# Kernel optimization log

Measured on AMD Instinct MI355X. Metric: run time of the kernel, lower is better.

Reference implementation:

```python
import jax, jax.numpy as jnp
import numpy as np

IN_DIM, HID, MEM, OUT = 512, 1024, 1024, 512
BATCH = 4096
HIST = 5  # hist_steps hard-coded in MMU.__init__

_LINEARS = [("inpgate", IN_DIM, HID), ("rec_inpgate", OUT, HID), ("mem_inpgate", MEM, HID),
            ("inp", IN_DIM, HID), ("rec_inp", OUT, HID),
            ("readgate", IN_DIM, MEM), ("rec_readgate", OUT, MEM), ("mem_readgate", MEM, MEM),
            ("decoder", HID, MEM),
            ("writegate", IN_DIM, MEM), ("rec_writegate", OUT, MEM), ("mem_writegate", MEM, MEM),
            ("encoder", MEM, HID)]


def setup_inputs() -> dict:
    key = jax.random.key(0)
    ks = iter(jax.random.split(key, 2 * len(_LINEARS) + 4))
    d = {"input": jax.random.normal(next(ks), (IN_DIM, BATCH), jnp.float32)}
    for name, fin, fout in _LINEARS:
        bound = 1.0 / np.sqrt(fin)  # torch nn.Linear default init range
        d["W_" + name] = jax.random.uniform(next(ks), (fout, fin), jnp.float32, -bound, bound)
        d["b_" + name] = jax.random.uniform(next(ks), (fout,), jnp.float32, -bound, bound)
    d["w_hid_out"] = jax.random.uniform(next(ks), (OUT, MEM), jnp.float32)  # torch.rand
    return d


def reference(input, W_inpgate, b_inpgate, W_rec_inpgate, b_rec_inpgate,
              W_mem_inpgate, b_mem_inpgate, W_inp, b_inp, W_rec_inp, b_rec_inp,
              W_readgate, b_readgate, W_rec_readgate, b_rec_readgate,
              W_mem_readgate, b_mem_readgate, W_decoder, b_decoder,
              W_writegate, b_writegate, W_rec_writegate, b_rec_writegate,
              W_mem_writegate, b_mem_writegate, W_encoder, b_encoder, w_hid_out):
    B = input.shape[1]
    lin = lambda x, W, b: x @ W.T + b
    # fresh module: history is zeros except last slot = current input (transposed to [B, in])
    xs = jnp.concatenate([jnp.zeros((HIST - 1, B, IN_DIM), input.dtype), input.T[None]], axis=0)

    def step(carry, x):
        out, mem = carry  # [B, OUT], [B, MEM]
        block_inp = jax.nn.sigmoid(lin(x, W_inp, b_inp) + lin(out, W_rec_inp, b_rec_inp))
        inp_gate = jax.nn.sigmoid(lin(x, W_inpgate, b_inpgate) + lin(mem, W_mem_inpgate, b_mem_inpgate)
                                  + lin(out, W_rec_inpgate, b_rec_inpgate))
        read_gate = jax.nn.sigmoid(lin(x, W_readgate, b_readgate) + lin(mem, W_mem_readgate, b_mem_readgate)
                                   + lin(out, W_rec_readgate, b_rec_readgate))
        decoded_mem = lin(read_gate * mem, W_decoder, b_decoder)
        hidden = decoded_mem + block_inp * inp_gate  # [B, HID] (HID == MEM)
        write_gate = jax.nn.sigmoid(lin(x, W_writegate, b_writegate) + lin(mem, W_mem_writegate, b_mem_writegate)
                                    + lin(out, W_rec_writegate, b_rec_writegate))
        encoded = jnp.tanh(lin(hidden, W_encoder, b_encoder))
        mem = (1.0 - write_gate) * mem + write_gate * encoded
        out = hidden @ w_hid_out.T  # w_hid_out.mm(hidden.T).T
        return (out, mem), None

    init = (jnp.zeros((B, OUT), input.dtype), jnp.zeros((B, MEM), input.dtype))
    (out, _mem), _ = jax.lax.scan(step, init, xs)
    return out
```

## Files before the change

### kernel.cpp

```cpp
#include <hip/hip_runtime.h>
#include <hip/hip_bf16.h>
#include <math.h>

typedef __hip_bfloat16 bf16;
typedef __attribute__((ext_vector_type(8))) short s16x8;
typedef __attribute__((ext_vector_type(4))) float f32x4;

__device__ __forceinline__ float sigf(float x) { return 1.0f / (1.0f + expf(-x)); }
__device__ __forceinline__ float dot4(float4 a, float4 b) {
  return a.x * b.x + a.y * b.y + a.z * b.z + a.w * b.w;
}

__global__ void setup(const float* __restrict__ W_inp, const float* __restrict__ W_ig,
                      const float* __restrict__ W_rg, const float* __restrict__ W_ho,
                      const float* __restrict__ W_dec, const float* __restrict__ input,
                      const float* __restrict__ b_inp, const float* __restrict__ b_rinp,
                      const float* __restrict__ b_ig, const float* __restrict__ b_mig,
                      const float* __restrict__ b_rig, const float* __restrict__ b_wg,
                      const float* __restrict__ b_mwg, const float* __restrict__ b_rwg,
                      const float* __restrict__ b_dec, bf16* __restrict__ Wcat,
                      bf16* __restrict__ WhoB, bf16* __restrict__ Wcat2, bf16* __restrict__ Wdt,
                      bf16* __restrict__ Xb, float* __restrict__ out_s, float* __restrict__ mem_s,
                      float* __restrict__ hidv, float* __restrict__ wgv) {
  __shared__ float t[32][33];
  const int id = blockIdx.x, tid = threadIdx.x;
  if (id < 8198) {
    const int i = id * 256 + tid;
    if (i < 524288) {
      Wcat[i] = __float2bfloat16(W_inp[i]);
    } else if (i < 1048576) {
      Wcat[i] = __float2bfloat16(W_ig[i - 524288]);
    } else if (i < 1572864) {
      Wcat[i] = __float2bfloat16(W_rg[i - 1048576]);
    } else if (i < 2097152) {
      const int k = i - 1572864;
      const bf16 vv = __float2bfloat16(W_ho[k]);
      WhoB[k] = vv;
      Wcat2[(size_t)(k >> 10) * 2048 + (k & 1023)] = vv;
    } else if (i < 2098688) {
      const int tt = i - 2097152;
      if (tt < 512) out_s[tt] = 0.0f;
      else mem_s[tt - 512] = 0.0f;
    }
  } else if (id < 10246) {
    const int b = id - 8198;
    const int i0 = (b >> 7) * 32, b0 = (b & 127) * 32;
    const int tx = tid & 31, ty = tid >> 5;
#pragma unroll
    for (int r = ty; r < 32; r += 8) t[r][tx] = input[(size_t)(i0 + r) * 4096 + b0 + tx];
    __syncthreads();
#pragma unroll
    for (int r = ty; r < 32; r += 8)
      Xb[(size_t)(b0 + r) * 512 + i0 + tx] = __float2bfloat16(t[tx][r]);
  } else if (id < 11270) {
    const int b = id - 10246;
    const int j0 = (b >> 5) * 32, k0 = (b & 31) * 32;
    const int tx = tid & 31, ty = tid >> 5;
#pragma unroll
    for (int r = ty; r < 32; r += 8) t[r][tx] = W_dec[(size_t)(j0 + r) * 1024 + k0 + tx];
    __syncthreads();
#pragma unroll
    for (int r = ty; r < 32; r += 8)
      Wdt[(size_t)(k0 + r) * 1024 + j0 + tx] = __float2bfloat16(t[tx][r]);
  } else {
    const int j = (id - 11270) * 256 + tid;
    const float bi = sigf(b_inp[j] + b_rinp[j]);
    const float ig = sigf(b_ig[j] + b_mig[j] + b_rig[j]);
    hidv[j] = b_dec[j] + bi * ig;
    wgv[j] = sigf(b_wg[j] + b_mwg[j] + b_rwg[j]);
  }
}

__global__ void step_gates(const float* __restrict__ Wri, const float* __restrict__ Wmig,
                           const float* __restrict__ Wrig, const float* __restrict__ Wmrg,
                           const float* __restrict__ Wrrg, const float* __restrict__ Wmwg,
                           const float* __restrict__ Wrwg, const float* __restrict__ b_inp,
                           const float* __restrict__ b_rinp, const float* __restrict__ b_ig,
                           const float* __restrict__ b_mig, const float* __restrict__ b_rig,
                           const float* __restrict__ b_rg, const float* __restrict__ b_mrg,
                           const float* __restrict__ b_rrg, const float* __restrict__ b_wg,
                           const float* __restrict__ b_mwg, const float* __restrict__ b_rwg,
                           const float* __restrict__ out_s, const float* __restrict__ mem_s,
                           float* __restrict__ rgm, float* __restrict__ h0v,
                           float* __restrict__ wgv) {
  __shared__ float red[7][4];
  const int j = blockIdx.x, tid = threadIdx.x, lane = tid & 63, wave = tid >> 6;
  const float4 z = make_float4(0.f, 0.f, 0.f, 0.f);
  const float4 o4 = (tid < 128) ? *(const float4*)(out_s + tid * 4) : z;
  const float4 m4 = *(const float4*)(mem_s + tid * 4);
  float p[7];
  p[0] = dot4((tid < 128) ? *(const float4*)(Wri + (size_t)j * 512 + tid * 4) : z, o4);
  p[1] = dot4(*(const float4*)(Wmig + (size_t)j * 1024 + tid * 4), m4);
  p[2] = dot4((tid < 128) ? *(const float4*)(Wrig + (size_t)j * 512 + tid * 4) : z, o4);
  p[3] = dot4(*(const float4*)(Wmrg + (size_t)j * 1024 + tid * 4), m4);
  p[4] = dot4((tid < 128) ? *(const float4*)(Wrrg + (size_t)j * 512 + tid * 4) : z, o4);
  p[5] = dot4(*(const float4*)(Wmwg + (size_t)j * 1024 + tid * 4), m4);
  p[6] = dot4((tid < 128) ? *(const float4*)(Wrwg + (size_t)j * 512 + tid * 4) : z, o4);
#pragma unroll
  for (int d = 0; d < 7; ++d) {
    float s = p[d];
#pragma unroll
    for (int off = 32; off > 0; off >>= 1) s += __shfl_down(s, off, 64);
    if (lane == 0) red[d][wave] = s;
  }
  __syncthreads();
  if (tid == 0) {
    float D[7];
#pragma unroll
    for (int d = 0; d < 7; ++d) D[d] = red[d][0] + red[d][1] + red[d][2] + red[d][3];
    const float abi = b_inp[j] + b_rinp[j] + D[0];
    const float aig = b_ig[j] + b_mig[j] + b_rig[j] + D[1] + D[2];
    const float arg = b_rg[j] + b_mrg[j] + b_rrg[j] + D[3] + D[4];
    const float awg = b_wg[j] + b_mwg[j] + b_rwg[j] + D[5] + D[6];
    rgm[j] = sigf(arg) * mem_s[j];
    h0v[j] = sigf(abi) * sigf(aig);
    wgv[j] = sigf(awg);
  }
}

__global__ void step_decode(const float* __restrict__ Wdec, const float* __restrict__ b_dec,
                            const float* __restrict__ rgm, const float* __restrict__ h0v,
                            float* __restrict__ hidv) {
  __shared__ float red[4];
  const int j = blockIdx.x, tid = threadIdx.x;
  const float4 a = *(const float4*)(Wdec + (size_t)j * 1024 + tid * 4);
  const float4 b = *(const float4*)(rgm + tid * 4);
  float s = dot4(a, b);
#pragma unroll
  for (int off = 32; off > 0; off >>= 1) s += __shfl_down(s, off, 64);
  if ((tid & 63) == 0) red[tid >> 6] = s;
  __syncthreads();
  if (tid == 0) hidv[j] = b_dec[j] + red[0] + red[1] + red[2] + red[3] + h0v[j];
}

__global__ void step_update(const float* __restrict__ Wenc, const float* __restrict__ b_enc,
                            const float* __restrict__ Who, const float* __restrict__ hidv,
                            const float* __restrict__ wgv, float* __restrict__ mem_s,
                            float* __restrict__ out_s) {
  __shared__ float red[4];
  const int id = blockIdx.x, tid = threadIdx.x;
  const float* row = (id < 1024) ? (Wenc + (size_t)id * 1024) : (Who + (size_t)(id - 1024) * 1024);
  const float4 a = *(const float4*)(row + tid * 4);
  const float4 b = *(const float4*)(hidv + tid * 4);
  float s = dot4(a, b);
#pragma unroll
  for (int off = 32; off > 0; off >>= 1) s += __shfl_down(s, off, 64);
  if ((tid & 63) == 0) red[tid >> 6] = s;
  __syncthreads();
  if (tid == 0) {
    const float d = red[0] + red[1] + red[2] + red[3];
    if (id < 1024) {
      const float wg = wgv[id];
      mem_s[id] = (1.0f - wg) * mem_s[id] + wg * tanhf(b_enc[id] + d);
    } else {
      out_s[id - 1024] = d;
    }
  }
}

__global__ void final_consts(const float* __restrict__ Wri, const float* __restrict__ Wmig,
                             const float* __restrict__ Wrig, const float* __restrict__ Wmrg,
                             const float* __restrict__ Wrrg, const float* __restrict__ b_inp,
                             const float* __restrict__ b_rinp, const float* __restrict__ b_ig,
                             const float* __restrict__ b_mig, const float* __restrict__ b_rig,
                             const float* __restrict__ b_rg, const float* __restrict__ b_mrg,
                             const float* __restrict__ b_rrg, const float* __restrict__ b_dec,
                             const float* __restrict__ Who, const float* __restrict__ out_s,
                             const float* __restrict__ mem_s, const float* __restrict__ P,
                             float* __restrict__ ccat, float* __restrict__ vout,
                             bf16* __restrict__ Wcat2) {
  __shared__ float red[5][4];
  const int id = blockIdx.x, tid = threadIdx.x, lane = tid & 63, wave = tid >> 6;
  if (id < 1024) {
    const float4 z = make_float4(0.f, 0.f, 0.f, 0.f);
    const float4 o4 = (tid < 128) ? *(const float4*)(out_s + tid * 4) : z;
    const float4 m4 = *(const float4*)(mem_s + tid * 4);
    float p[5];
    p[0] = dot4((tid < 128) ? *(const float4*)(Wri + (size_t)id * 512 + tid * 4) : z, o4);
    p[1] = dot4(*(const float4*)(Wmig + (size_t)id * 1024 + tid * 4), m4);
    p[2] = dot4((tid < 128) ? *(const float4*)(Wrig + (size_t)id * 512 + tid * 4) : z, o4);
    p[3] = dot4(*(const float4*)(Wmrg + (size_t)id * 1024 + tid * 4), m4);
    p[4] = dot4((tid < 128) ? *(const float4*)(Wrrg + (size_t)id * 512 + tid * 4) : z, o4);
#pragma unroll
    for (int d = 0; d < 5; ++d) {
      float s = p[d];
#pragma unroll
      for (int off = 32; off > 0; off >>= 1) s += __shfl_down(s, off, 64);
      if (lane == 0) red[d][wave] = s;
    }
    __syncthreads();
    if (tid == 0) {
      float D[5];
#pragma unroll
      for (int d = 0; d < 5; ++d) D[d] = red[d][0] + red[d][1] + red[d][2] + red[d][3];
      ccat[id] = b_inp[id] + b_rinp[id] + D[0];
      ccat[1024 + id] = b_ig[id] + b_mig[id] + b_rig[id] + D[1] + D[2];
      ccat[2048 + id] = b_rg[id] + b_mrg[id] + b_rrg[id] + D[3] + D[4];
    }
  } else if (id < 1536) {
    const int o = id - 1024;
    const float4 a = *(const float4*)(Who + (size_t)o * 1024 + tid * 4);
    const float4 b = *(const float4*)(b_dec + tid * 4);
    float s = dot4(a, b);
#pragma unroll
    for (int off = 32; off > 0; off >>= 1) s += __shfl_down(s, off, 64);
    if (lane == 0) red[0][wave] = s;
    __syncthreads();
    if (tid == 0) vout[o] = red[0][0] + red[0][1] + red[0][2] + red[0][3];
  } else {
    const int idx = (id - 1536) * 256 + tid;
    const int q = idx >> 10, k = idx & 1023;
    Wcat2[(size_t)q * 2048 + 1024 + k] = __float2bfloat16(P[idx] * mem_s[k]);
  }
}

__global__ void combine(const bf16* __restrict__ Gbi, const bf16* __restrict__ Gig,
                        bf16* __restrict__ Hcat) {
  const int i = blockIdx.x * 256 + threadIdx.x;
  const size_t idx8 = (size_t)i * 8;
  const int b = i >> 7;
  const int j = (int)(idx8 & 1023);
  const s16x8 x = *(const s16x8*)(Gbi + idx8);
  const s16x8 y = *(const s16x8*)(Gig + idx8);
  s16x8 o;
#pragma unroll
  for (int t = 0; t < 8; ++t) {
    const float fx = __bfloat162float(((const bf16*)&x)[t]);
    const float fy = __bfloat162float(((const bf16*)&y)[t]);
    ((bf16*)&o)[t] = __float2bfloat16(fx * fy);
  }
  *(s16x8*)(Hcat + (size_t)b * 2048 + j) = o;
}

template <int BM, int BN, int EPI>
__global__ __launch_bounds__(256, 3) void gemm_bt(const bf16* __restrict__ A,
                                                  const bf16* __restrict__ Bp, const int K,
                                                  const float* __restrict__ cvec,
                                                  bf16* __restrict__ pb0, bf16* __restrict__ pb1,
                                                  bf16* __restrict__ pb2, float* __restrict__ pf) {
  constexpr int IM = BM / 32, JN = BN / 32;
  __shared__ bf16 smem[(BM + BN) * 64];
  const int tid = threadIdx.x, wave = tid >> 6, lane = tid & 63;
  const int wm = wave >> 1, wn = wave & 1;
  const int m0 = blockIdx.y * BM, n0 = blockIdx.x * BN;
  f32x4 acc[IM][JN] = {};

  for (int kt = 0; kt < K; kt += 64) {
    __syncthreads();
#pragma unroll
    for (int i = 0; i < BM / 32; ++i) {
      const int ci = i * 256 + tid;
      const int row = ci >> 3, sck = ci & 7, ck = sck ^ (row & 7);
      const bf16* g = A + (size_t)(m0 + row) * K + kt + ck * 8;
      const unsigned lofs = (unsigned)__builtin_amdgcn_readfirstlane((i * 256 + wave * 64) * 16);
      __builtin_amdgcn_global_load_lds(
          (const __attribute__((address_space(1))) void*)g,
          (__attribute__((address_space(3))) void*)((char*)smem + lofs), 16, 0, 0);
    }
#pragma unroll
    for (int i = 0; i < BN / 32; ++i) {
      const int ci = i * 256 + tid;
      const int row = ci >> 3, sck = ci & 7, ck = sck ^ (row & 7);
      const bf16* g = Bp + (size_t)(n0 + row) * K + kt + ck * 8;
      const unsigned lofs =
          (unsigned)__builtin_amdgcn_readfirstlane(BM * 128 + (i * 256 + wave * 64) * 16);
      __builtin_amdgcn_global_load_lds(
          (const __attribute__((address_space(1))) void*)g,
          (__attribute__((address_space(3))) void*)((char*)smem + lofs), 16, 0, 0);
    }
    __syncthreads();

#pragma unroll
    for (int ks = 0; ks < 2; ++ks) {
      const int ckk = ks * 4 + (lane >> 4);
      s16x8 af[IM];
#pragma unroll
      for (int i = 0; i < IM; ++i) {
        const int R = wm * (BM / 2) + i * 16 + (lane & 15);
        af[i] = *(const s16x8*)((const char*)smem + (R * 8 + (ckk ^ (R & 7))) * 16);
      }
#pragma unroll
      for (int j = 0; j < JN; ++j) {
        const int R = wn * (BN / 2) + j * 16 + (lane & 15);
        const s16x8 bfr =
            *(const s16x8*)((const char*)smem + BM * 128 + (R * 8 + (ckk ^ (R & 7))) * 16);
#pragma unroll
        for (int i = 0; i < IM; ++i)
          acc[i][j] = __builtin_amdgcn_mfma_f32_16x16x32_bf16(af[i], bfr, acc[i][j], 0, 0, 0);
      }
    }
  }

  const int mb = (lane >> 4) * 4, nb = lane & 15;
#pragma unroll
  for (int i = 0; i < IM; ++i) {
#pragma unroll
    for (int j = 0; j < JN; ++j) {
      const int col = n0 + wn * (BN / 2) + j * 16 + nb;
#pragma unroll
      for (int r = 0; r < 4; ++r) {
        const int rowg = m0 + wm * (BM / 2) + i * 16 + mb + r;
        const float v = acc[i][j][r];
        if (EPI == 0) {
          pf[(size_t)rowg * 1024 + col] = v;
        } else if (EPI == 1) {
          const float s = sigf(v + cvec[col]);
          const int g = col >> 10, jj = col & 1023;
          if (g == 0) pb0[(size_t)rowg * 1024 + jj] = __float2bfloat16(s);
          else if (g == 1) pb1[(size_t)rowg * 1024 + jj] = __float2bfloat16(s);
          else pb2[(size_t)rowg * 2048 + 1024 + jj] = __float2bfloat16(s);
        } else {
          pf[(size_t)rowg * 512 + col] = v + cvec[col];
        }
      }
    }
  }
}

extern "C" void kernel_launch(void* const* d_in, const int* in_sizes, int n_in, void* d_out,
                              int out_size, void* d_ws, size_t ws_size, hipStream_t stream) {
  const float* input  = (const float*)d_in[0];
  const float* W_ig   = (const float*)d_in[1];  const float* b_ig   = (const float*)d_in[2];
  const float* W_rig  = (const float*)d_in[3];  const float* b_rig  = (const float*)d_in[4];
  const float* W_mig  = (const float*)d_in[5];  const float* b_mig  = (const float*)d_in[6];
  const float* W_inp  = (const float*)d_in[7];  const float* b_inp  = (const float*)d_in[8];
  const float* W_rinp = (const float*)d_in[9];  const float* b_rinp = (const float*)d_in[10];
  const float* W_rg   = (const float*)d_in[11]; const float* b_rg   = (const float*)d_in[12];
  const float* W_rrg  = (const float*)d_in[13]; const float* b_rrg  = (const float*)d_in[14];
  const float* W_mrg  = (const float*)d_in[15]; const float* b_mrg  = (const float*)d_in[16];
  const float* W_dec  = (const float*)d_in[17]; const float* b_dec  = (const float*)d_in[18];
  const float* W_wg   = (const float*)d_in[19]; const float* b_wg   = (const float*)d_in[20];
  const float* W_rwg  = (const float*)d_in[21]; const float* b_rwg  = (const float*)d_in[22];
  const float* W_mwg  = (const float*)d_in[23]; const float* b_mwg  = (const float*)d_in[24];
  const float* W_enc  = (const float*)d_in[25]; const float* b_enc  = (const float*)d_in[26];
  const float* W_ho   = (const float*)d_in[27];
  (void)W_wg; (void)W_rwg; (void)W_mwg;

  char* ws = (char*)d_ws;
  float* out_s = (float*)(ws + 0);
  float* mem_s = (float*)(ws + 4096);
  float* rgm   = (float*)(ws + 8192);
  float* h0v   = (float*)(ws + 12288);
  float* wgv   = (float*)(ws + 16384);
  float* hidv  = (float*)(ws + 20480);
  float* ccat  = (float*)(ws + 24576);
  float* vout  = (float*)(ws + 36864);
  float* P     = (float*)(ws + 65536);
  bf16* Xb     = (bf16*)(ws + 2162688);
  bf16* Wcat   = (bf16*)(ws + 6356992);
  bf16* WhoB   = (bf16*)(ws + 9502720);
  bf16* Wcat2  = (bf16*)(ws + 10551296);
  bf16* Wdt    = (bf16*)(ws + 12648448);
  bf16* Gbi    = (bf16*)(ws + 14745600);
  bf16* Gig    = (bf16*)(ws + 23134208);
  bf16* Hcat   = (bf16*)(ws + 31522816);

  setup<<<11274, 256, 0, stream>>>(W_inp, W_ig, W_rg, W_ho, W_dec, input, b_inp, b_rinp, b_ig,
                                   b_mig, b_rig, b_wg, b_mwg, b_rwg, b_dec, Wcat, WhoB, Wcat2,
                                   Wdt, Xb, out_s, mem_s, hidv, wgv);

  gemm_bt<64, 64, 0><<<dim3(16, 8), 256, 0, stream>>>(WhoB, Wdt, 1024, nullptr, nullptr, nullptr,
                                                      nullptr, P);

  step_update<<<1536, 256, 0, stream>>>(W_enc, b_enc, W_ho, hidv, wgv, mem_s, out_s);

  for (int s = 0; s < 3; ++s) {
    step_gates<<<1024, 256, 0, stream>>>(W_rinp, W_mig, W_rig, W_mrg, W_rrg, W_mwg, W_rwg, b_inp,
                                         b_rinp, b_ig, b_mig, b_rig, b_rg, b_mrg, b_rrg, b_wg,
                                         b_mwg, b_rwg, out_s, mem_s, rgm, h0v, wgv);
    step_decode<<<1024, 256, 0, stream>>>(W_dec, b_dec, rgm, h0v, hidv);
    step_update<<<1536, 256, 0, stream>>>(W_enc, b_enc, W_ho, hidv, wgv, mem_s, out_s);
  }

  final_consts<<<3584, 256, 0, stream>>>(W_rinp, W_mig, W_rig, W_mrg, W_rrg, b_inp, b_rinp, b_ig,
                                         b_mig, b_rig, b_rg, b_mrg, b_rrg, b_dec, W_ho, out_s,
                                         mem_s, P, ccat, vout, Wcat2);

  gemm_bt<128, 128, 1><<<dim3(24, 32), 256, 0, stream>>>(Xb, Wcat, 512, ccat, Gbi, Gig, Hcat,
                                                         nullptr);
  combine<<<2048, 256, 0, stream>>>(Gbi, Gig, Hcat);

  gemm_bt<64, 64, 2><<<dim3(8, 64), 256, 0, stream>>>(Hcat, Wcat2, 2048, vout, nullptr, nullptr,
                                                      nullptr, (float*)d_out);
}
```

Measured before the change: 245.5 us.

## Fuse gate GEMMs with combine epilogue and split-K final GEMM via atomics

Replaces the three-gate GEMM plus a separate combine kernel with one GEMM that computes all three gate tiles per block and writes the sigmoid products and read gate straight into Hcat through an LDS-staged epilogue. The intermediate Gbi/Gig buffers go away. The P and output GEMMs become split-K kernels that atomically add into pre-initialised buffers, with the vout bias precomputed in setup and broadcast by a new out_init kernel. Sigmoid and tanh switch to fast exp/rcp intrinsics. This gives more parallelism for the small GEMMs, but float atomics make results nondeterministic and the fast math lowers accuracy.

```diff
diff --git a/kernel.cpp b/kernel.cpp
--- a/kernel.cpp
+++ b/kernel.cpp
@@ -6,7 +6,10 @@
 typedef __attribute__((ext_vector_type(8))) short s16x8;
 typedef __attribute__((ext_vector_type(4))) float f32x4;
 
-__device__ __forceinline__ float sigf(float x) { return 1.0f / (1.0f + expf(-x)); }
+__device__ __forceinline__ float fsig(float x) {
+  return __builtin_amdgcn_rcpf(1.0f + __expf(-x));
+}
+__device__ __forceinline__ float ftanh(float x) { return 2.0f * fsig(2.0f * x) - 1.0f; }
 __device__ __forceinline__ float dot4(float4 a, float4 b) {
   return a.x * b.x + a.y * b.y + a.z * b.z + a.w * b.w;
 }
@@ -21,7 +24,8 @@
                       const float* __restrict__ b_dec, bf16* __restrict__ Wcat,
                       bf16* __restrict__ WhoB, bf16* __restrict__ Wcat2, bf16* __restrict__ Wdt,
                       bf16* __restrict__ Xb, float* __restrict__ out_s, float* __restrict__ mem_s,
-                      float* __restrict__ hidv, float* __restrict__ wgv) {
+                      float* __restrict__ hidv, float* __restrict__ wgv, float* __restrict__ P,
+                      float* __restrict__ vout) {
   __shared__ float t[32][33];
   const int id = blockIdx.x, tid = threadIdx.x;
   if (id < 8198) {
@@ -62,13 +66,31 @@
 #pragma unroll
     for (int r = ty; r < 32; r += 8)
       Wdt[(size_t)(k0 + r) * 1024 + j0 + tx] = __float2bfloat16(t[tx][r]);
+  } else if (id < 11274) {
+    const int j = (id - 11270) * 256 + tid;
+    const float bi = fsig(b_inp[j] + b_rinp[j]);
+    const float ig = fsig(b_ig[j] + b_mig[j] + b_rig[j]);
+    hidv[j] = b_dec[j] + bi * ig;
+    wgv[j] = fsig(b_wg[j] + b_mwg[j] + b_rwg[j]);
+  } else if (id < 11786) {
+    const int i = (id - 11274) * 256 + tid;
+    ((float4*)P)[i] = make_float4(0.f, 0.f, 0.f, 0.f);
   } else {
-    const int j = (id - 11270) * 256 + tid;
-    const float bi = sigf(b_inp[j] + b_rinp[j]);
-    const float ig = sigf(b_ig[j] + b_mig[j] + b_rig[j]);
-    hidv[j] = b_dec[j] + bi * ig;
-    wgv[j] = sigf(b_wg[j] + b_mwg[j] + b_rwg[j]);
-  }
+    const int o = id - 11786;
+    const float4 a = *(const float4*)(W_ho + (size_t)o * 1024 + tid * 4);
+    const float4 b = *(const float4*)(b_dec + tid * 4);
+    float s = dot4(a, b);
+#pragma unroll
+    for (int off = 32; off > 0; off >>= 1) s += __shfl_down(s, off, 64);
+    if ((tid & 63) == 0) t[0][tid >> 6] = s;
+    __syncthreads();
+    if (tid == 0) vout[o] = t[0][0] + t[0][1] + t[0][2] + t[0][3];
+  }
+}
+
+__global__ void out_init(const float* __restrict__ vout, float* __restrict__ out) {
+  const int i = blockIdx.x * 256 + threadIdx.x;
+  ((float4*)out)[i] = ((const float4*)vout)[i & 127];
 }
 
 __global__ void step_gates(const float* __restrict__ Wri, const float* __restrict__ Wmig,
@@ -112,9 +134,9 @@
     const float aig = b_ig[j] + b_mig[j] + b_rig[j] + D[1] + D[2];
     const float arg = b_rg[j] + b_mrg[j] + b_rrg[j] + D[3] + D[4];
     const float awg = b_wg[j] + b_mwg[j] + b_rwg[j] + D[5] + D[6];
-    rgm[j] = sigf(arg) * mem_s[j];
-    h0v[j] = sigf(abi) * sigf(aig);
-    wgv[j] = sigf(awg);
+    rgm[j] = fsig(arg) * mem_s[j];
+    h0v[j] = fsig(abi) * fsig(aig);
+    wgv[j] = fsig(awg);
   }
 }
 
@@ -151,7 +173,7 @@
     const float d = red[0] + red[1] + red[2] + red[3];
     if (id < 1024) {
       const float wg = wgv[id];
-      mem_s[id] = (1.0f - wg) * mem_s[id] + wg * tanhf(b_enc[id] + d);
+      mem_s[id] = (1.0f - wg) * mem_s[id] + wg * ftanh(b_enc[id] + d);
     } else {
       out_s[id - 1024] = d;
     }
@@ -164,11 +186,9 @@
                              const float* __restrict__ b_rinp, const float* __restrict__ b_ig,
                              const float* __restrict__ b_mig, const float* __restrict__ b_rig,
                              const float* __restrict__ b_rg, const float* __restrict__ b_mrg,
-                             const float* __restrict__ b_rrg, const float* __restrict__ b_dec,
-                             const float* __restrict__ Who, const float* __restrict__ out_s,
+                             const float* __restrict__ b_rrg, const float* __restrict__ out_s,
                              const float* __restrict__ mem_s, const float* __restrict__ P,
-                             float* __restrict__ ccat, float* __restrict__ vout,
-                             bf16* __restrict__ Wcat2) {
+                             float* __restrict__ ccat, bf16* __restrict__ Wcat2) {
   __shared__ float red[5][4];
   const int id = blockIdx.x, tid = threadIdx.x, lane = tid & 63, wave = tid >> 6;
   if (id < 1024) {
@@ -197,95 +217,161 @@
       ccat[1024 + id] = b_ig[id] + b_mig[id] + b_rig[id] + D[1] + D[2];
       ccat[2048 + id] = b_rg[id] + b_mrg[id] + b_rrg[id] + D[3] + D[4];
     }
-  } else if (id < 1536) {
-    const int o = id - 1024;
-    const float4 a = *(const float4*)(Who + (size_t)o * 1024 + tid * 4);
-    const float4 b = *(const float4*)(b_dec + tid * 4);
-    float s = dot4(a, b);
-#pragma unroll
-    for (int off = 32; off > 0; off >>= 1) s += __shfl_down(s, off, 64);
-    if (lane == 0) red[0][wave] = s;
-    __syncthreads();
-    if (tid == 0) vout[o] = red[0][0] + red[0][1] + red[0][2] + red[0][3];
   } else {
-    const int idx = (id - 1536) * 256 + tid;
+    const int idx = (id - 1024) * 256 + tid;
     const int q = idx >> 10, k = idx & 1023;
     Wcat2[(size_t)q * 2048 + 1024 + k] = __float2bfloat16(P[idx] * mem_s[k]);
   }
 }
 
-__global__ void combine(const bf16* __restrict__ Gbi, const bf16* __restrict__ Gig,
-                        bf16* __restrict__ Hcat) {
-  const int i = blockIdx.x * 256 + threadIdx.x;
-  const size_t idx8 = (size_t)i * 8;
-  const int b = i >> 7;
-  const int j = (int)(idx8 & 1023);
-  const s16x8 x = *(const s16x8*)(Gbi + idx8);
-  const s16x8 y = *(const s16x8*)(Gig + idx8);
-  s16x8 o;
-#pragma unroll
-  for (int t = 0; t < 8; ++t) {
-    const float fx = __bfloat162float(((const bf16*)&x)[t]);
-    const float fy = __bfloat162float(((const bf16*)&y)[t]);
-    ((bf16*)&o)[t] = __float2bfloat16(fx * fy);
-  }
-  *(s16x8*)(Hcat + (size_t)b * 2048 + j) = o;
-}
-
-template <int BM, int BN, int EPI>
-__global__ __launch_bounds__(256, 3) void gemm_bt(const bf16* __restrict__ A,
-                                                  const bf16* __restrict__ Bp, const int K,
-                                                  const float* __restrict__ cvec,
-                                                  bf16* __restrict__ pb0, bf16* __restrict__ pb1,
-                                                  bf16* __restrict__ pb2, float* __restrict__ pf) {
-  constexpr int IM = BM / 32, JN = BN / 32;
-  __shared__ bf16 smem[(BM + BN) * 64];
+__global__ __launch_bounds__(256) void gemm_gates(const bf16* __restrict__ A,
+                                                  const bf16* __restrict__ Wcat,
+                                                  const float* __restrict__ ccat,
+                                                  bf16* __restrict__ Hcat) {
+  __shared__ char smem[57344];
   const int tid = threadIdx.x, wave = tid >> 6, lane = tid & 63;
   const int wm = wave >> 1, wn = wave & 1;
-  const int m0 = blockIdx.y * BM, n0 = blockIdx.x * BN;
-  f32x4 acc[IM][JN] = {};
-
-  for (int kt = 0; kt < K; kt += 64) {
-    __syncthreads();
-#pragma unroll
-    for (int i = 0; i < BM / 32; ++i) {
+  const int m0 = blockIdx.y * 64, n0 = blockIdx.x * 128;
+  f32x4 acc[3][2][4] = {};
+
+  for (int kt = 0; kt < 512; kt += 64) {
+    __syncthreads();
+#pragma unroll
+    for (int i = 0; i < 2; ++i) {
       const int ci = i * 256 + tid;
-      const int row = ci >> 3, sck = ci & 7, ck = sck ^ (row & 7);
-      const bf16* g = A + (size_t)(m0 + row) * K + kt + ck * 8;
+      const int row = ci >> 3, ck = (ci & 7) ^ (row & 7);
+      const bf16* g = A + (size_t)(m0 + row) * 512 + kt + ck * 8;
       const unsigned lofs = (unsigned)__builtin_amdgcn_readfirstlane((i * 256 + wave * 64) * 16);
       __builtin_amdgcn_global_load_lds(
           (const __attribute__((address_space(1))) void*)g,
-          (__attribute__((address_space(3))) void*)((char*)smem + lofs), 16, 0, 0);
-    }
-#pragma unroll
-    for (int i = 0; i < BN / 32; ++i) {
+          (__attribute__((address_space(3))) void*)(smem + lofs), 16, 0, 0);
+    }
+#pragma unroll
+    for (int gI = 0; gI < 3; ++gI) {
+      const bf16* Bp = Wcat + gI * 524288;
+#pragma unroll
+      for (int i = 0; i < 4; ++i) {
+        const int ci = i * 256 + tid;
+        const int row = ci >> 3, ck = (ci & 7) ^ (row & 7);
+        const bf16* g = Bp + (size_t)(n0 + row) * 512 + kt + ck * 8;
+        const unsigned lofs = (unsigned)__builtin_amdgcn_readfirstlane(
+            8192 + gI * 16384 + (i * 256 + wave * 64) * 16);
+        __builtin_amdgcn_global_load_lds(
+            (const __attribute__((address_space(1))) void*)g,
+            (__attribute__((address_space(3))) void*)(smem + lofs), 16, 0, 0);
+      }
+    }
+    __syncthreads();
+
+#pragma unroll
+    for (int ks = 0; ks < 2; ++ks) {
+      const int ckk = ks * 4 + (lane >> 4);
+      s16x8 af[2];
+#pragma unroll
+      for (int i = 0; i < 2; ++i) {
+        const int R = wm * 32 + i * 16 + (lane & 15);
+        af[i] = *(const s16x8*)(smem + (R * 8 + (ckk ^ (R & 7))) * 16);
+      }
+#pragma unroll
+      for (int gI = 0; gI < 3; ++gI) {
+#pragma unroll
+        for (int j = 0; j < 4; ++j) {
+          const int R = wn * 64 + j * 16 + (lane & 15);
+          const s16x8 bfr =
+              *(const s16x8*)(smem + 8192 + gI * 16384 + (R * 8 + (ckk ^ (R & 7))) * 16);
+#pragma unroll
+          for (int i = 0; i < 2; ++i)
+            acc[gI][i][j] =
+                __builtin_amdgcn_mfma_f32_16x16x32_bf16(af[i], bfr, acc[gI][i][j], 0, 0, 0);
+        }
+      }
+    }
+  }
+
+  __syncthreads();
+  bf16* sm = (bf16*)smem;
+  bf16* sr = (bf16*)smem + 8704;
+  const int mb = (lane >> 4) * 4, nb = lane & 15;
+#pragma unroll
+  for (int i = 0; i < 2; ++i) {
+#pragma unroll
+    for (int j = 0; j < 4; ++j) {
+      const int colL = wn * 64 + j * 16 + nb;
+      const int jg = n0 + colL;
+      const float c0 = ccat[jg], c1 = ccat[1024 + jg], c2 = ccat[2048 + jg];
+#pragma unroll
+      for (int r = 0; r < 4; ++r) {
+        const int rowL = wm * 32 + i * 16 + mb + r;
+        const float h = fsig(acc[0][i][j][r] + c0) * fsig(acc[1][i][j][r] + c1);
+        const float rg = fsig(acc[2][i][j][r] + c2);
+        sm[rowL * 136 + colL] = __float2bfloat16(h);
+        sr[rowL * 136 + colL] = __float2bfloat16(rg);
+      }
+    }
+  }
+  __syncthreads();
+#pragma unroll
+  for (int p = 0; p < 4; ++p) {
+    const int c = p * 256 + tid;
+    const int row = c >> 4, cc = c & 15;
+    const s16x8 v0 = *(const s16x8*)(sm + row * 136 + cc * 8);
+    const s16x8 v1 = *(const s16x8*)(sr + row * 136 + cc * 8);
+    *(s16x8*)(Hcat + (size_t)(m0 + row) * 2048 + n0 + cc * 8) = v0;
+    *(s16x8*)(Hcat + (size_t)(m0 + row) * 2048 + 1024 + n0 + cc * 8) = v1;
+  }
+}
+
+__global__ __launch_bounds__(256) void gemm_at(const bf16* __restrict__ A,
+                                               const bf16* __restrict__ Bp, const int Ktot,
+                                               const int kspan, const int ldout,
+                                               float* __restrict__ outF) {
+  __shared__ char smem[24576];
+  const int tid = threadIdx.x, wave = tid >> 6, lane = tid & 63;
+  const int wm = wave >> 1, wn = wave & 1;
+  const int m0 = blockIdx.y * 64, n0 = blockIdx.x * 128;
+  const int kt0 = blockIdx.z * kspan;
+  f32x4 acc[2][4] = {};
+
+  for (int kt = kt0; kt < kt0 + kspan; kt += 64) {
+    __syncthreads();
+#pragma unroll
+    for (int i = 0; i < 2; ++i) {
       const int ci = i * 256 + tid;
-      const int row = ci >> 3, sck = ci & 7, ck = sck ^ (row & 7);
-      const bf16* g = Bp + (size_t)(n0 + row) * K + kt + ck * 8;
-      const unsigned lofs =
-          (unsigned)__builtin_amdgcn_readfirstlane(BM * 128 + (i * 256 + wave * 64) * 16);
+      const int row = ci >> 3, ck = (ci & 7) ^ (row & 7);
+      const bf16* g = A + (size_t)(m0 + row) * Ktot + kt + ck * 8;
+      const unsigned lofs = (unsigned)__builtin_amdgcn_readfirstlane((i * 256 + wave * 64) * 16);
       __builtin_amdgcn_global_load_lds(
           (const __attribute__((address_space(1))) void*)g,
-          (__attribute__((address_space(3))) void*)((char*)smem + lofs), 16, 0, 0);
+          (__attribute__((address_space(3))) void*)(smem + lofs), 16, 0, 0);
+    }
+#pragma unroll
+    for (int i = 0; i < 4; ++i) {
+      const int ci = i * 256 + tid;
+      const int row = ci >> 3, ck = (ci & 7) ^ (row & 7);
+      const bf16* g = Bp + (size_t)(n0 + row) * Ktot + kt + ck * 8;
+      const unsigned lofs =
+          (unsigned)__builtin_amdgcn_readfirstlane(8192 + (i * 256 + wave * 64) * 16);
+      __builtin_amdgcn_global_load_lds(
+          (const __attribute__((address_space(1))) void*)g,
+          (__attribute__((address_space(3))) void*)(smem + lofs), 16, 0, 0);
     }
     __syncthreads();
 
 #pragma unroll
     for (int ks = 0; ks < 2; ++ks) {
       const int ckk = ks * 4 + (lane >> 4);
-      s16x8 af[IM];
-#pragma unroll
-      for (int i = 0; i < IM; ++i) {
-        const int R = wm * (BM / 2) + i * 16 + (lane & 15);
-        af[i] = *(const s16x8*)((const char*)smem + (R * 8 + (ckk ^ (R & 7))) * 16);
-      }
-#pragma unroll
-      for (int j = 0; j < JN; ++j) {
-        const int R = wn * (BN / 2) + j * 16 + (lane & 15);
-        const s16x8 bfr =
-            *(const s16x8*)((const char*)smem + BM * 128 + (R * 8 + (ckk ^ (R & 7))) * 16);
-#pragma unroll
-        for (int i = 0; i < IM; ++i)
+      s16x8 af[2];
+#pragma unroll
+      for (int i = 0; i < 2; ++i) {
+        const int R = wm * 32 + i * 16 + (lane & 15);
+        af[i] = *(const s16x8*)(smem + (R * 8 + (ckk ^ (R & 7))) * 16);
+      }
+#pragma unroll
+      for (int j = 0; j < 4; ++j) {
+        const int R = wn * 64 + j * 16 + (lane & 15);
+        const s16x8 bfr = *(const s16x8*)(smem + 8192 + (R * 8 + (ckk ^ (R & 7))) * 16);
+#pragma unroll
+        for (int i = 0; i < 2; ++i)
           acc[i][j] = __builtin_amdgcn_mfma_f32_16x16x32_bf16(af[i], bfr, acc[i][j], 0, 0, 0);
       }
     }
@@ -293,25 +379,14 @@
 
   const int mb = (lane >> 4) * 4, nb = lane & 15;
 #pragma unroll
-  for (int i = 0; i < IM; ++i) {
-#pragma unroll
-    for (int j = 0; j < JN; ++j) {
-      const int col = n0 + wn * (BN / 2) + j * 16 + nb;
+  for (int i = 0; i < 2; ++i) {
+#pragma unroll
+    for (int j = 0; j < 4; ++j) {
+      const int col = n0 + wn * 64 + j * 16 + nb;
 #pragma unroll
       for (int r = 0; r < 4; ++r) {
-        const int rowg = m0 + wm * (BM / 2) + i * 16 + mb + r;
-        const float v = acc[i][j][r];
-        if (EPI == 0) {
-          pf[(size_t)rowg * 1024 + col] = v;
-        } else if (EPI == 1) {
-          const float s = sigf(v + cvec[col]);
-          const int g = col >> 10, jj = col & 1023;
-          if (g == 0) pb0[(size_t)rowg * 1024 + jj] = __float2bfloat16(s);
-          else if (g == 1) pb1[(size_t)rowg * 1024 + jj] = __float2bfloat16(s);
-          else pb2[(size_t)rowg * 2048 + 1024 + jj] = __float2bfloat16(s);
-        } else {
-          pf[(size_t)rowg * 512 + col] = v + cvec[col];
-        }
+        const int rowg = m0 + wm * 32 + i * 16 + mb + r;
+        atomicAdd(outF + (size_t)rowg * ldout + col, acc[i][j][r]);
       }
     }
   }
@@ -344,23 +419,22 @@
   float* wgv   = (float*)(ws + 16384);
   float* hidv  = (float*)(ws + 20480);
   float* ccat  = (float*)(ws + 24576);
-  float* vout  = (float*)(ws + 36864);
+  float* vout  = (float*)(ws + 40960);
   float* P     = (float*)(ws + 65536);
   bf16* Xb     = (bf16*)(ws + 2162688);
   bf16* Wcat   = (bf16*)(ws + 6356992);
   bf16* WhoB   = (bf16*)(ws + 9502720);
   bf16* Wcat2  = (bf16*)(ws + 10551296);
   bf16* Wdt    = (bf16*)(ws + 12648448);
-  bf16* Gbi    = (bf16*)(ws + 14745600);
-  bf16* Gig    = (bf16*)(ws + 23134208);
-  bf16* Hcat   = (bf16*)(ws + 31522816);
-
-  setup<<<11274, 256, 0, stream>>>(W_inp, W_ig, W_rg, W_ho, W_dec, input, b_inp, b_rinp, b_ig,
+  bf16* Hcat   = (bf16*)(ws + 14745600);
+
+  setup<<<12298, 256, 0, stream>>>(W_inp, W_ig, W_rg, W_ho, W_dec, input, b_inp, b_rinp, b_ig,
                                    b_mig, b_rig, b_wg, b_mwg, b_rwg, b_dec, Wcat, WhoB, Wcat2,
-                                   Wdt, Xb, out_s, mem_s, hidv, wgv);
-
-  gemm_bt<64, 64, 0><<<dim3(16, 8), 256, 0, stream>>>(WhoB, Wdt, 1024, nullptr, nullptr, nullptr,
-                                                      nullptr, P);
+                                   Wdt, Xb, out_s, mem_s, hidv, wgv, P, vout);
+
+  gemm_at<<<dim3(8, 8, 4), 256, 0, stream>>>(WhoB, Wdt, 1024, 256, 1024, P);
+
+  out_init<<<2048, 256, 0, stream>>>(vout, (float*)d_out);
 
   step_update<<<1536, 256, 0, stream>>>(W_enc, b_enc, W_ho, hidv, wgv, mem_s, out_s);
 
@@ -372,14 +446,11 @@
     step_update<<<1536, 256, 0, stream>>>(W_enc, b_enc, W_ho, hidv, wgv, mem_s, out_s);
   }
 
-  final_consts<<<3584, 256, 0, stream>>>(W_rinp, W_mig, W_rig, W_mrg, W_rrg, b_inp, b_rinp, b_ig,
-                                         b_mig, b_rig, b_rg, b_mrg, b_rrg, b_dec, W_ho, out_s,
-                                         mem_s, P, ccat, vout, Wcat2);
-
-  gemm_bt<128, 128, 1><<<dim3(24, 32), 256, 0, stream>>>(Xb, Wcat, 512, ccat, Gbi, Gig, Hcat,
-                                                         nullptr);
-  combine<<<2048, 256, 0, stream>>>(Gbi, Gig, Hcat);
-
-  gemm_bt<64, 64, 2><<<dim3(8, 64), 256, 0, stream>>>(Hcat, Wcat2, 2048, vout, nullptr, nullptr,
-                                                      nullptr, (float*)d_out);
-}
+  final_consts<<<3072, 256, 0, stream>>>(W_rinp, W_mig, W_rig, W_mrg, W_rrg, b_inp, b_rinp, b_ig,
+                                         b_mig, b_rig, b_rg, b_mrg, b_rrg, out_s, mem_s, P, ccat,
+                                         Wcat2);
+
+  gemm_gates<<<dim3(8, 64), 256, 0, stream>>>(Xb, Wcat, ccat, Hcat);
+
+  gemm_at<<<dim3(4, 64, 2), 256, 0, stream>>>(Hcat, Wcat2, 2048, 1024, 512, (float*)d_out);
+}
```

Result: no change. 246.2 us (+0.3%).
